# Optimization experiments

Hardware: AMD Instinct MI355X
Metric: run time of the kernel (lower is better)

The kernel has to match this reference:

```python
import jax, jax.numpy as jnp
import numpy as np

N_NODES = 100000
N_EDGES = 1600000
IN_C = 16
OUT_C = 16
N_EATTR = 8


def setup_inputs() -> dict:
    key = jax.random.key(0)
    k1, k2, k3, k4 = jax.random.split(key, 4)
    x = jax.random.normal(k1, (N_NODES, IN_C), dtype=jnp.float32)
    edge_index = jax.random.randint(k2, (2, N_EDGES), 0, N_NODES, dtype=jnp.int64)
    edge_attr = jax.random.normal(k3, (N_EDGES, N_EATTR), dtype=jnp.float32)
    # learned params (original inits to ones/zeros; use small random for a non-degenerate baseline)
    weight_matrix = jax.random.normal(k4, (N_EATTR, OUT_C, IN_C), dtype=jnp.float32) * 0.1
    bias = jnp.zeros((OUT_C,), dtype=jnp.float32)
    return {
        "x": x,
        "edge_index": edge_index,
        "edge_attr": edge_attr,
        "weight_matrix": weight_matrix,
        "bias": bias,
        "num_nodes": N_NODES,
    }


def reference(x, edge_index, edge_attr, weight_matrix, bias, num_nodes):
    # message: per-edge weight W_e = edge_attr @ weight_matrix (-> [E, out, in]),
    # then msg_e = W_e @ x[src_e]. Fused in one einsum to avoid the [E,out,in] blow-up.
    src = edge_index[0]
    dst = edge_index[1]
    x_j = x[src]                                   # [E, in]
    msg = jnp.einsum('ea,aoi,ei->eo', edge_attr, weight_matrix, x_j)  # [E, out]
    # aggregate: scatter-add messages to destination nodes
    aggr = jax.ops.segment_sum(msg, dst, num_segments=num_nodes)      # [N, out]
    # update: bias + relu
    return jax.nn.relu(aggr + bias)
```

## Files before the change

kernel.cpp:

```cpp
#include <hip/hip_runtime.h>


#define IN_C 16
#define OUT_C 16
#define NA 8

typedef unsigned short u16;

__device__ __forceinline__ float bfbits(unsigned hi) {
    union { unsigned u; float f; } c; c.u = hi; return c.f;
}
__device__ __forceinline__ u16 f2bf(float f) {
    union { float f; unsigned u; } c; c.f = f;
    unsigned u = c.u + (0x7fffu + ((c.u >> 16) & 1u));
    return (u16)(u >> 16);
}

__global__ void __launch_bounds__(256) k_stage1(
    const float* __restrict__ x, const float* __restrict__ W,
    const int* __restrict__ ei, long long n_edges,
    u16* __restrict__ y, int* __restrict__ flag, int n_nodes) {
    __shared__ int s_nz;
    if (blockIdx.x == 0) {
        if (threadIdx.x == 0) s_nz = 0;
        __syncthreads();
        long long lim = 2 * n_edges;
        long long step = (n_edges / 256) | 1;
        long long pos = 1 + 2 * (long long)threadIdx.x * step;
        if (pos < lim && ei[pos] != 0) atomicOr(&s_nz, 1);
        __syncthreads();
        if (threadIdx.x == 0) flag[0] = (s_nz == 0) ? 1 : 0;
    }

    __shared__ float Wl[OUT_C][129];
    for (int k = threadIdx.x; k < NA * OUT_C * IN_C; k += 256) {
        int a = k >> 8, o = (k >> 4) & 15, i = k & 15;
        Wl[o][a * IN_C + i] = W[k];
    }
    __syncthreads();

    int idx = blockIdx.x * 256 + threadIdx.x;
    if (idx >= n_nodes * OUT_C) return;
    int n = idx >> 4, o = idx & 15;
    const float4* xp = reinterpret_cast<const float4*>(x + (size_t)n * IN_C);
    float4 x0 = xp[0], x1 = xp[1], x2 = xp[2], x3 = xp[3];
    float xv[16] = {x0.x, x0.y, x0.z, x0.w, x1.x, x1.y, x1.z, x1.w,
                    x2.x, x2.y, x2.z, x2.w, x3.x, x3.y, x3.z, x3.w};
    float acc[NA];
#pragma unroll
    for (int a = 0; a < NA; ++a) {
        float s = 0.f;
#pragma unroll
        for (int i = 0; i < IN_C; ++i) s = fmaf(Wl[o][a * IN_C + i], xv[i], s);
        acc[a] = s;
    }
    union { uint4 u; u16 h[8]; } pk;
#pragma unroll
    for (int a = 0; a < NA; ++a) pk.h[a] = f2bf(acc[a]);
    reinterpret_cast<uint4*>(y + ((size_t)n * OUT_C + o) * NA)[0] = pk.u;
}

__global__ void __launch_bounds__(256) k_stage2(
    const int* __restrict__ ei, const float* __restrict__ ea,
    const u16* __restrict__ y, float* __restrict__ out,
    const int* __restrict__ flag, long long n_edges) {
    long long idx = (long long)blockIdx.x * 256 + threadIdx.x;
    if (idx >= n_edges * OUT_C) return;
    long long e = idx >> 4;
    int o = (int)(idx & 15);
    int src, dst;
    if (flag[0]) { src = ei[2 * e]; dst = ei[2 * (n_edges + e)]; }
    else         { src = ei[e];     dst = ei[n_edges + e]; }

    const float4* ap = reinterpret_cast<const float4*>(ea + e * NA);
    float4 a0 = ap[0], a1 = ap[1];
    uint4 yu = reinterpret_cast<const uint4*>(y + ((size_t)src * OUT_C + o) * NA)[0];

    float s =      bfbits(yu.x << 16)        * a0.x;
    s = fmaf(bfbits(yu.x & 0xffff0000u), a0.y, s);
    s = fmaf(bfbits(yu.y << 16),         a0.z, s);
    s = fmaf(bfbits(yu.y & 0xffff0000u), a0.w, s);
    s = fmaf(bfbits(yu.z << 16),         a1.x, s);
    s = fmaf(bfbits(yu.z & 0xffff0000u), a1.y, s);
    s = fmaf(bfbits(yu.w << 16),         a1.z, s);
    s = fmaf(bfbits(yu.w & 0xffff0000u), a1.w, s);

    unsafeAtomicAdd(out + (size_t)dst * OUT_C + o, s);
}

__global__ void __launch_bounds__(256) k_direct(
    const float* __restrict__ x, const int* __restrict__ ei,
    const float* __restrict__ ea, const float* __restrict__ W,
    float* __restrict__ out, long long n_edges) {
    __shared__ float Wl[OUT_C][129];
    for (int k = threadIdx.x; k < NA * OUT_C * IN_C; k += 256) {
        int a = k >> 8, o = (k >> 4) & 15, i = k & 15;
        Wl[o][a * IN_C + i] = W[k];
    }
    __syncthreads();
    long long idx = (long long)blockIdx.x * 256 + threadIdx.x;
    if (idx >= n_edges * OUT_C) return;
    long long e = idx >> 4;
    int o = (int)(idx & 15);
    int src = ei[2 * e], dst = ei[2 * (n_edges + e)];
    const float4* ap = reinterpret_cast<const float4*>(ea + e * NA);
    float4 a0 = ap[0], a1 = ap[1];
    float av[NA] = {a0.x, a0.y, a0.z, a0.w, a1.x, a1.y, a1.z, a1.w};
    const float4* xp = reinterpret_cast<const float4*>(x + (size_t)src * IN_C);
    float4 x0 = xp[0], x1 = xp[1], x2 = xp[2], x3 = xp[3];
    float xv[16] = {x0.x, x0.y, x0.z, x0.w, x1.x, x1.y, x1.z, x1.w,
                    x2.x, x2.y, x2.z, x2.w, x3.x, x3.y, x3.z, x3.w};
    float s = 0.f;
#pragma unroll
    for (int a = 0; a < NA; ++a) {
        float d = 0.f;
#pragma unroll
        for (int i = 0; i < IN_C; ++i) d = fmaf(Wl[o][a * IN_C + i], xv[i], d);
        s = fmaf(av[a], d, s);
    }
    unsafeAtomicAdd(out + (size_t)dst * OUT_C + o, s);
}

__global__ void __launch_bounds__(256) k_bias_relu(
    const float* __restrict__ bias, float* __restrict__ out, int total4) {
    int idx = blockIdx.x * 256 + threadIdx.x;
    if (idx >= total4) return;
    int j0 = (idx & 3) * 4;
    const float4 b = reinterpret_cast<const float4*>(bias + j0)[0];
    float4* op = reinterpret_cast<float4*>(out) + idx;
    float4 v = op[0];
    v.x = fmaxf(v.x + b.x, 0.f);
    v.y = fmaxf(v.y + b.y, 0.f);
    v.z = fmaxf(v.z + b.z, 0.f);
    v.w = fmaxf(v.w + b.w, 0.f);
    op[0] = v;
}

extern "C" void kernel_launch(void* const* d_in, const int* in_sizes, int n_in,
                              void* d_out, int out_size, void* d_ws, size_t ws_size,
                              hipStream_t stream) {
    const float* x    = (const float*)d_in[0];
    const int*   ei   = (const int*)d_in[1];
    const float* ea   = (const float*)d_in[2];
    const float* W    = (const float*)d_in[3];
    const float* bias = (const float*)d_in[4];
    float* out = (float*)d_out;

    int n_nodes = in_sizes[0] / IN_C;
    long long n_edges = in_sizes[2] / NA;

    hipMemsetAsync(d_out, 0, (size_t)n_nodes * OUT_C * sizeof(float), stream);

    long long tE = n_edges * OUT_C;
    int gE = (int)((tE + 255) / 256);

    size_t y_bytes = (size_t)n_nodes * OUT_C * NA * sizeof(u16);
    if (ws_size >= 64 + y_bytes) {
        int* flag = (int*)d_ws;
        u16* y = (u16*)((char*)d_ws + 64);
        int t1 = n_nodes * OUT_C;
        k_stage1<<<(t1 + 255) / 256, 256, 0, stream>>>(x, W, ei, n_edges, y, flag, n_nodes);
        k_stage2<<<gE, 256, 0, stream>>>(ei, ea, y, out, flag, n_edges);
    } else {
        k_direct<<<gE, 256, 0, stream>>>(x, ei, ea, W, out, n_edges);
    }

    int t4 = (n_nodes * OUT_C) / 4;
    k_bias_relu<<<(t4 + 255) / 256, 256, 0, stream>>>(bias, out, t4);
}
```

Before: 220.5 us.

## Give each thread four outputs per edge, two nodes per thread, fold zeroing in

```diff
diff --git a/kernel.cpp b/kernel.cpp
--- a/kernel.cpp
+++ b/kernel.cpp
@@ -15,11 +15,19 @@
     unsigned u = c.u + (0x7fffu + ((c.u >> 16) & 1u));
     return (u16)(u >> 16);
 }
+__device__ __forceinline__ float dot4(float4 a, float4 b) {
+    float s = a.x * b.x;
+    s = fmaf(a.y, b.y, s);
+    s = fmaf(a.z, b.z, s);
+    s = fmaf(a.w, b.w, s);
+    return s;
+}
 
 __global__ void __launch_bounds__(256) k_stage1(
     const float* __restrict__ x, const float* __restrict__ W,
     const int* __restrict__ ei, long long n_edges,
-    u16* __restrict__ y, int* __restrict__ flag, int n_nodes) {
+    u16* __restrict__ y, float* __restrict__ out,
+    int* __restrict__ flag, int n_nodes) {
     __shared__ int s_nz;
     if (blockIdx.x == 0) {
         if (threadIdx.x == 0) s_nz = 0;
@@ -32,60 +40,82 @@
         if (threadIdx.x == 0) flag[0] = (s_nz == 0) ? 1 : 0;
     }
 
-    __shared__ float Wl[OUT_C][129];
-    for (int k = threadIdx.x; k < NA * OUT_C * IN_C; k += 256) {
-        int a = k >> 8, o = (k >> 4) & 15, i = k & 15;
-        Wl[o][a * IN_C + i] = W[k];
+    __shared__ float4 Wl[OUT_C][33];
+    for (int k = threadIdx.x; k < 512; k += 256) {
+        int a = k >> 6, o = (k >> 2) & 15, q = k & 3;
+        Wl[o][a * 4 + q] = reinterpret_cast<const float4*>(W)[k];
     }
     __syncthreads();
 
+    int npairs = (n_nodes + 1) >> 1;
     int idx = blockIdx.x * 256 + threadIdx.x;
-    if (idx >= n_nodes * OUT_C) return;
-    int n = idx >> 4, o = idx & 15;
-    const float4* xp = reinterpret_cast<const float4*>(x + (size_t)n * IN_C);
-    float4 x0 = xp[0], x1 = xp[1], x2 = xp[2], x3 = xp[3];
-    float xv[16] = {x0.x, x0.y, x0.z, x0.w, x1.x, x1.y, x1.z, x1.w,
-                    x2.x, x2.y, x2.z, x2.w, x3.x, x3.y, x3.z, x3.w};
-    float acc[NA];
+    if (idx >= npairs * OUT_C) return;
+    int p = idx >> 4, o = idx & 15;
+    int n0 = p * 2;
+    bool has1 = (n0 + 1) < n_nodes;
+
+    const float4* xp0 = reinterpret_cast<const float4*>(x + (size_t)n0 * IN_C);
+    float4 X0[4] = {xp0[0], xp0[1], xp0[2], xp0[3]};
+    float4 X1[4];
+    if (has1) {
+        const float4* xp1 = reinterpret_cast<const float4*>(x + (size_t)(n0 + 1) * IN_C);
+        X1[0] = xp1[0]; X1[1] = xp1[1]; X1[2] = xp1[2]; X1[3] = xp1[3];
+    }
+
+    union { uint4 u; u16 h[8]; } pk0, pk1;
 #pragma unroll
     for (int a = 0; a < NA; ++a) {
-        float s = 0.f;
-#pragma unroll
-        for (int i = 0; i < IN_C; ++i) s = fmaf(Wl[o][a * IN_C + i], xv[i], s);
-        acc[a] = s;
+        float4 w0 = Wl[o][a * 4 + 0], w1 = Wl[o][a * 4 + 1];
+        float4 w2 = Wl[o][a * 4 + 2], w3 = Wl[o][a * 4 + 3];
+        float s0 = dot4(w0, X0[0]) + dot4(w1, X0[1]) + dot4(w2, X0[2]) + dot4(w3, X0[3]);
+        pk0.h[a] = f2bf(s0);
+        if (has1) {
+            float s1 = dot4(w0, X1[0]) + dot4(w1, X1[1]) + dot4(w2, X1[2]) + dot4(w3, X1[3]);
+            pk1.h[a] = f2bf(s1);
+        }
     }
-    union { uint4 u; u16 h[8]; } pk;
-#pragma unroll
-    for (int a = 0; a < NA; ++a) pk.h[a] = f2bf(acc[a]);
-    reinterpret_cast<uint4*>(y + ((size_t)n * OUT_C + o) * NA)[0] = pk.u;
+    reinterpret_cast<uint4*>(y + ((size_t)n0 * OUT_C + o) * NA)[0] = pk0.u;
+    out[(size_t)n0 * OUT_C + o] = 0.f;
+    if (has1) {
+        reinterpret_cast<uint4*>(y + ((size_t)(n0 + 1) * OUT_C + o) * NA)[0] = pk1.u;
+        out[(size_t)(n0 + 1) * OUT_C + o] = 0.f;
+    }
 }
 
 __global__ void __launch_bounds__(256) k_stage2(
     const int* __restrict__ ei, const float* __restrict__ ea,
     const u16* __restrict__ y, float* __restrict__ out,
     const int* __restrict__ flag, long long n_edges) {
-    long long idx = (long long)blockIdx.x * 256 + threadIdx.x;
-    if (idx >= n_edges * OUT_C) return;
-    long long e = idx >> 4;
-    int o = (int)(idx & 15);
+    long long gid = (long long)blockIdx.x * 256 + threadIdx.x;
+    if (gid >= n_edges * 4) return;
+    long long e = gid >> 2;
+    int q = (int)(gid & 3);
     int src, dst;
     if (flag[0]) { src = ei[2 * e]; dst = ei[2 * (n_edges + e)]; }
     else         { src = ei[e];     dst = ei[n_edges + e]; }
 
     const float4* ap = reinterpret_cast<const float4*>(ea + e * NA);
     float4 a0 = ap[0], a1 = ap[1];
-    uint4 yu = reinterpret_cast<const uint4*>(y + ((size_t)src * OUT_C + o) * NA)[0];
+    float av[NA] = {a0.x, a0.y, a0.z, a0.w, a1.x, a1.y, a1.z, a1.w};
 
-    float s =      bfbits(yu.x << 16)        * a0.x;
-    s = fmaf(bfbits(yu.x & 0xffff0000u), a0.y, s);
-    s = fmaf(bfbits(yu.y << 16),         a0.z, s);
-    s = fmaf(bfbits(yu.y & 0xffff0000u), a0.w, s);
-    s = fmaf(bfbits(yu.z << 16),         a1.x, s);
-    s = fmaf(bfbits(yu.z & 0xffff0000u), a1.y, s);
-    s = fmaf(bfbits(yu.w << 16),         a1.z, s);
-    s = fmaf(bfbits(yu.w & 0xffff0000u), a1.w, s);
-
-    unsafeAtomicAdd(out + (size_t)dst * OUT_C + o, s);
+    const uint4* yp = reinterpret_cast<const uint4*>(y + ((size_t)src * OUT_C + q * 4) * NA);
+    float s[4];
+#pragma unroll
+    for (int j = 0; j < 4; ++j) {
+        uint4 yu = yp[j];
+        float t = bfbits(yu.x << 16) * av[0];
+        t = fmaf(bfbits(yu.x & 0xffff0000u), av[1], t);
+        t = fmaf(bfbits(yu.y << 16),         av[2], t);
+        t = fmaf(bfbits(yu.y & 0xffff0000u), av[3], t);
+        t = fmaf(bfbits(yu.z << 16),         av[4], t);
+        t = fmaf(bfbits(yu.z & 0xffff0000u), av[5], t);
+        t = fmaf(bfbits(yu.w << 16),         av[6], t);
+        t = fmaf(bfbits(yu.w & 0xffff0000u), av[7], t);
+        s[j] = t;
+    }
+    float* op = out + (size_t)dst * OUT_C + q * 4;
+#pragma unroll
+    for (int j = 0; j < 4; ++j) unsafeAtomicAdd(op + j, s[j]);
 }
 
 __global__ void __launch_bounds__(256) k_direct(
@@ -149,20 +179,19 @@
     int n_nodes = in_sizes[0] / IN_C;
     long long n_edges = in_sizes[2] / NA;
 
-    hipMemsetAsync(d_out, 0, (size_t)n_nodes * OUT_C * sizeof(float), stream);
-
-    long long tE = n_edges * OUT_C;
-    int gE = (int)((tE + 255) / 256);
-
     size_t y_bytes = (size_t)n_nodes * OUT_C * NA * sizeof(u16);
     if (ws_size >= 64 + y_bytes) {
         int* flag = (int*)d_ws;
         u16* y = (u16*)((char*)d_ws + 64);
-        int t1 = n_nodes * OUT_C;
-        k_stage1<<<(t1 + 255) / 256, 256, 0, stream>>>(x, W, ei, n_edges, y, flag, n_nodes);
-        k_stage2<<<gE, 256, 0, stream>>>(ei, ea, y, out, flag, n_edges);
+        int npairs = (n_nodes + 1) >> 1;
+        int t1 = npairs * OUT_C;
+        k_stage1<<<(t1 + 255) / 256, 256, 0, stream>>>(x, W, ei, n_edges, y, out, flag, n_nodes);
+        long long tE = n_edges * 4;
+        k_stage2<<<(int)((tE + 255) / 256), 256, 0, stream>>>(ei, ea, y, out, flag, n_edges);
     } else {
-        k_direct<<<gE, 256, 0, stream>>>(x, ei, ea, W, out, n_edges);
+        hipMemsetAsync(d_out, 0, (size_t)n_nodes * OUT_C * sizeof(float), stream);
+        long long tE = n_edges * OUT_C;
+        k_direct<<<(int)((tE + 255) / 256), 256, 0, stream>>>(x, ei, ea, W, out, n_edges);
     }
 
     int t4 = (n_nodes * OUT_C) / 4;
```

Measured after the change: 438.5 us. 98.9% more time.
